# Performance work log

Hardware: AMD Instinct MI355X
Metric: run time of the kernel (lower is better)

Reference implementation:

```python
import jax, jax.numpy as jnp
import numpy as np

B, H, D, S = 128, 64, 96, 256  # batch, heads, head_dim, num cache slots


def setup_inputs() -> dict:
    key = jax.random.key(0)
    k0, k1, k2, k3, k4, k5 = jax.random.split(key, 6)
    return {
        "q": jax.random.normal(k0, (B, H, 1, D), dtype=jnp.float32),
        "k": jax.random.normal(k1, (B, H, 1, D), dtype=jnp.float32),
        "v": jax.random.normal(k2, (B, H, 1, D), dtype=jnp.float32),
        "kv_caches": jax.random.normal(k3, (S, H, D, D), dtype=jnp.float32),
        "slope_rate": jax.random.uniform(k4, (H,), dtype=jnp.float32),
        "slot_idx": jax.random.randint(k5, (B,), 0, S, dtype=jnp.int32),
    }


def reference(q, k, v, kv_caches, slope_rate, slot_idx):
    # q/k/v: [B,H,1,D] -> [B,H,D]
    q3, k3, v3 = q[:, :, 0], k[:, :, 0], v[:, :, 0]
    valid = slot_idx >= 0                                   # [B]
    safe_slot = jnp.where(valid, slot_idx, 0)
    ratio = jnp.exp(-slope_rate)                            # [H] decay per head
    kv_old = kv_caches[safe_slot]                           # gather: [B,H,D,D]
    # decayed outer-product state update: kv_new = k v^T + exp(-slope)*kv_old
    kv_new = k3[..., :, None] * v3[..., None, :] + ratio[None, :, None, None] * kv_old
    # fused reduce: out[b,h,e] = sum_d q[b,h,d] * kv_new[b,h,d,e]
    out = jnp.einsum('bhd,bhde->bhe', q3, kv_new)
    out = jnp.where(valid[:, None, None], out, 0.0)         # slot_id == -1 -> zeros
    return out[:, :, None, :]                               # [B,H,1,D]
```

## Files before the change

kernel.cpp:

```cpp
#include <hip/hip_runtime.h>


#define NB 128
#define NH 64
#define ND 96
#define NS 256

__global__ __launch_bounds__(128, 4) void la_decode(
    const float* __restrict__ q, const float* __restrict__ k,
    const float* __restrict__ v, const float* __restrict__ kvc,
    const float* __restrict__ slope, const int* __restrict__ slot_idx,
    float* __restrict__ out)
{
    const int bid = blockIdx.x;
    const int h = bid >> 7;
    const int b = bid & (NB - 1);
    const int t = threadIdx.x;

    __shared__ float qs[ND];
    __shared__ float red[128];
    __shared__ float part[4][ND];

    const int slot = slot_idx[b];
    const bool valid = slot >= 0;
    const int safe = valid ? slot : 0;

    const int bh = b * NH + h;

    float p = 0.f;
    if (t < ND) {
        float qv = q[bh * ND + t];
        qs[t] = qv;
        p = qv * k[bh * ND + t];
    }
    red[t] = p;
    __syncthreads();

    #pragma unroll
    for (int s = 64; s > 0; s >>= 1) {
        if (t < s) red[t] += red[t + s];
        __syncthreads();
    }
    const float qk = red[0];

    float4 acc = make_float4(0.f, 0.f, 0.f, 0.f);
    if (t < 96) {
        const int dp = t / 24;
        const int e4 = t % 24;
        const float* __restrict__ kp =
            kvc + ((size_t)safe * NH + h) * (size_t)(ND * ND);
        const float4* __restrict__ kp4 = (const float4*)(kp + 4 * t);
        #pragma unroll 8
        for (int j = 0; j < 24; ++j) {
            const float4 kv4 = kp4[j * 96];
            const float qd = qs[j * 4 + dp];
            acc.x = fmaf(qd, kv4.x, acc.x);
            acc.y = fmaf(qd, kv4.y, acc.y);
            acc.z = fmaf(qd, kv4.z, acc.z);
            acc.w = fmaf(qd, kv4.w, acc.w);
        }
        *(float4*)&part[dp][e4 * 4] = acc;
    }
    __syncthreads();

    if (t < ND) {
        const float dot = part[0][t] + part[1][t] + part[2][t] + part[3][t];
        const float ratio = __expf(-slope[h]);
        const float o = valid ? fmaf(qk, v[bh * ND + t], ratio * dot) : 0.f;
        out[bh * ND + t] = o;
    }
}

extern "C" void kernel_launch(void* const* d_in, const int* in_sizes, int n_in,
                              void* d_out, int out_size, void* d_ws, size_t ws_size,
                              hipStream_t stream) {
    const float* q     = (const float*)d_in[0];
    const float* k     = (const float*)d_in[1];
    const float* v     = (const float*)d_in[2];
    const float* kvc   = (const float*)d_in[3];
    const float* slope = (const float*)d_in[4];
    const int*   slot  = (const int*)d_in[5];
    float* out = (float*)d_out;

    dim3 grid(NB * NH);
    dim3 block(128);
    la_decode<<<grid, block, 0, stream>>>(q, k, v, kvc, slope, slot, out);
}
```

Baseline: 700.7 us.

## Spread KV-tile loads across all 128 threads and use wave shuffle reduction

The q·k dot product now uses a wavefront shuffle-xor reduction instead of a shared-memory tree with repeated barriers. The 96x96 state tile is read by all 128 threads, each doing 18 float4 loads, where before 96 threads each did 24. Each thread keeps three accumulators selected by column phase, and a 16-way shared-memory reduction replaces the 4-way one. This raises memory-level parallelism and cuts barrier count, but makes the final reduction larger and the indexing more complex.

Result: no change. 703.1 us (+0.3%).

```diff
diff --git a/kernel.cpp b/kernel.cpp
--- a/kernel.cpp
+++ b/kernel.cpp
@@ -18,56 +18,70 @@
     const int t = threadIdx.x;
 
     __shared__ float qs[ND];
-    __shared__ float red[128];
-    __shared__ float part[4][ND];
+    __shared__ float red[2];
+    __shared__ float4 part[24][17];
 
     const int slot = slot_idx[b];
     const bool valid = slot >= 0;
     const int safe = valid ? slot : 0;
-
     const int bh = b * NH + h;
 
     float p = 0.f;
+    float vv = 0.f;
     if (t < ND) {
-        float qv = q[bh * ND + t];
+        const float qv = q[bh * ND + t];
         qs[t] = qv;
         p = qv * k[bh * ND + t];
+        vv = v[bh * ND + t];
     }
-    red[t] = p;
+    #pragma unroll
+    for (int m = 32; m > 0; m >>= 1) p += __shfl_xor(p, m, 64);
+    if ((t & 63) == 0) red[t >> 6] = p;
     __syncthreads();
 
+    const float4* __restrict__ kp4 =
+        (const float4*)(kvc + ((size_t)safe * NH + h) * (size_t)(ND * ND)) + t;
+
+    float4 acc[3];
+    acc[0] = make_float4(0.f, 0.f, 0.f, 0.f);
+    acc[1] = make_float4(0.f, 0.f, 0.f, 0.f);
+    acc[2] = make_float4(0.f, 0.f, 0.f, 0.f);
+
+    int d = t / 24;
+    int c = t % 24;
     #pragma unroll
-    for (int s = 64; s > 0; s >>= 1) {
-        if (t < s) red[t] += red[t + s];
-        __syncthreads();
+    for (int i = 0; i < 18; ++i) {
+        const float4 kv4 = kp4[(size_t)(128 * i)];
+        const float qd = qs[d];
+        float4& a = acc[i % 3];
+        a.x = fmaf(qd, kv4.x, a.x);
+        a.y = fmaf(qd, kv4.y, a.y);
+        a.z = fmaf(qd, kv4.z, a.z);
+        a.w = fmaf(qd, kv4.w, a.w);
+        const int ov = (c + 8) >= 24;
+        c = c + 8 - (ov ? 24 : 0);
+        d = d + 5 + ov;
     }
-    const float qk = red[0];
 
-    float4 acc = make_float4(0.f, 0.f, 0.f, 0.f);
-    if (t < 96) {
-        const int dp = t / 24;
-        const int e4 = t % 24;
-        const float* __restrict__ kp =
-            kvc + ((size_t)safe * NH + h) * (size_t)(ND * ND);
-        const float4* __restrict__ kp4 = (const float4*)(kp + 4 * t);
-        #pragma unroll 8
-        for (int j = 0; j < 24; ++j) {
-            const float4 kv4 = kp4[j * 96];
-            const float qd = qs[j * 4 + dp];
-            acc.x = fmaf(qd, kv4.x, acc.x);
-            acc.y = fmaf(qd, kv4.y, acc.y);
-            acc.z = fmaf(qd, kv4.z, acc.z);
-            acc.w = fmaf(qd, kv4.w, acc.w);
-        }
-        *(float4*)&part[dp][e4 * 4] = acc;
+    {
+        const int r  = t >> 3;
+        const int c0 = t % 24;
+        const int c1 = (c0 + 8)  % 24;
+        const int c2 = (c0 + 16) % 24;
+        part[c0][r] = acc[0];
+        part[c1][r] = acc[1];
+        part[c2][r] = acc[2];
     }
     __syncthreads();
 
     if (t < ND) {
-        const float dot = part[0][t] + part[1][t] + part[2][t] + part[3][t];
+        float dot = 0.f;
+        #pragma unroll
+        for (int rr = 0; rr < 16; ++rr)
+            dot += ((const float*)&part[t >> 2][rr])[t & 3];
+        const float qk = red[0] + red[1];
         const float ratio = __expf(-slope[h]);
-        const float o = valid ? fmaf(qk, v[bh * ND + t], ratio * dot) : 0.f;
-        out[bh * ND + t] = o;
+        out[bh * ND + t] = valid ? fmaf(qk, vv, ratio * dot) : 0.f;
     }
 }
 
```
